# Kernel optimization log

Hardware: AMD Instinct MI355X
Metric: run time of the kernel (lower is better)

Reference implementation:

```python
import jax, jax.numpy as jnp
import numpy as np

T, B, C, H = 2048, 2, 1024, 16
D = C // H
SCALE = D ** -0.5
WSTD = C ** -0.5  # keep activations O(1) so softmax is not saturated


def setup_inputs() -> dict:
    key = jax.random.key(0)
    ks = jax.random.split(key, 6)
    return {
        "x": jax.random.normal(ks[0], (T, B, C), dtype=jnp.float32),
        "wq": jax.random.normal(ks[1], (C, C), dtype=jnp.float32) * WSTD,
        "wk": jax.random.normal(ks[2], (C, C), dtype=jnp.float32) * WSTD,
        "wv": jax.random.normal(ks[3], (C, C), dtype=jnp.float32) * WSTD,
        "wo": jax.random.normal(ks[4], (C, C), dtype=jnp.float32) * WSTD,
        "bo": jax.random.normal(ks[5], (C,), dtype=jnp.float32) * 0.02,
    }


def reference(x, wq, wk, wv, wo, bo):
    t, b, c = x.shape
    x2 = x.reshape(t * b, c)
    # SelfAttentionLinears: q scaled by head_dim^-0.5 inside the addmm
    q = (x2 @ wq) * SCALE
    k = x2 @ wk
    v = x2 @ wv
    # fairseq layout: (T, B*H, D) -> (B*H, T, D)
    q = q.reshape(t, b * H, D).transpose(1, 0, 2)
    k = k.reshape(t, b * H, D).transpose(1, 0, 2)
    v = v.reshape(t, b * H, D).transpose(1, 0, 2)
    # strided_bmm1: scores [B*H, T, T]
    scores = jnp.einsum('bqd,bkd->bqk', q, k)
    attn = jax.nn.softmax(scores, axis=-1)
    # strided_bmm2: context [B*H, T, D]
    ctx = jnp.einsum('bqk,bkd->bqd', attn, v)
    out = ctx.transpose(1, 0, 2).reshape(t, b, c)
    return out @ wo + bo
```

## Files before the change

kernel.cpp:

```cpp
#include <hip/hip_runtime.h>
#include <math.h>

#define T_DIM 2048
#define B_DIM 2
#define C_DIM 1024
#define H_DIM 16
#define D_DIM 64
#define M_DIM (T_DIM * B_DIM)
#define SCALE_Q 0.125f

typedef short short8 __attribute__((ext_vector_type(8)));
typedef float f32x4  __attribute__((ext_vector_type(4)));
typedef unsigned short ushort_t;

__device__ __forceinline__ unsigned short f2bf(float f) {
    unsigned int u = __builtin_bit_cast(unsigned int, f);
    u += 0x7FFFu + ((u >> 16) & 1u);
    return (unsigned short)(u >> 16);
}

__device__ __forceinline__ void gl_lds16(const void* g, void* l) {
    __builtin_amdgcn_global_load_lds(
        (const __attribute__((address_space(1))) void*)g,
        (__attribute__((address_space(3))) void*)l, 16, 0, 0);
}

__global__ __launch_bounds__(256) void prep(
    const float* __restrict__ x,
    const float* __restrict__ wq, const float* __restrict__ wk,
    const float* __restrict__ wv, const float* __restrict__ wo,
    ushort_t* __restrict__ xb,
    ushort_t* __restrict__ wqkv_t, ushort_t* __restrict__ wo_t)
{
    __shared__ float tile[64][65];
    const int tid = threadIdx.x;
    const int z   = blockIdx.z;

    if (z == 4) {
        const size_t base =
            ((size_t)(blockIdx.y * 16 + blockIdx.x)) * 16384 + (size_t)tid * 8;
#pragma unroll
        for (int j = 0; j < 8; ++j) {
            const size_t i = base + (size_t)j * 2048;
            const float4 v0 = *(const float4*)&x[i];
            const float4 v1 = *(const float4*)&x[i + 4];
            ushort_t o[8] = {f2bf(v0.x), f2bf(v0.y), f2bf(v0.z), f2bf(v0.w),
                             f2bf(v1.x), f2bf(v1.y), f2bf(v1.z), f2bf(v1.w)};
            *(uint4*)&xb[i] = *(uint4*)o;
        }
        return;
    }

    const int k0 = blockIdx.x * 64;
    const int n0 = blockIdx.y * 64;
    const float* src = (z == 0) ? wq : (z == 1) ? wk : (z == 2) ? wv : wo;
    ushort_t* dst = (z < 3) ? (wqkv_t + (size_t)z * C_DIM * C_DIM) : wo_t;

    const int r = tid >> 4;
    const int c = (tid & 15) * 4;
#pragma unroll
    for (int i = 0; i < 4; ++i) {
        const float4 v = *(const float4*)&src[(size_t)(k0 + r + i * 16) * C_DIM + n0 + c];
        *(float4*)&tile[r + i * 16][c] = v;
    }
    __syncthreads();
#pragma unroll
    for (int i = 0; i < 4; ++i) {
        const int r2 = r + i * 16;
        ushort4 o;
        o.x = f2bf(tile[c + 0][r2]); o.y = f2bf(tile[c + 1][r2]);
        o.z = f2bf(tile[c + 2][r2]); o.w = f2bf(tile[c + 3][r2]);
        *(ushort4*)&dst[(size_t)(n0 + r2) * C_DIM + k0 + c] = o;
    }
}

__global__ __launch_bounds__(256) void qkv_mfma(
    const ushort_t* __restrict__ xb, const ushort_t* __restrict__ wt,
    ushort_t* __restrict__ q_ws, ushort_t* __restrict__ k_ws,
    ushort_t* __restrict__ v_ws)
{
    __shared__ ushort_t lds[18432];
    ushort_t* As = lds;
    ushort_t* Bs = lds + 4096;

    const int tid  = threadIdx.x;
    const int n0   = blockIdx.x * 128;
    const int m0   = blockIdx.y * 128;
    const int w    = tid >> 6;
    const int lane = tid & 63;
    const int l16  = lane & 15;
    const int quad = lane >> 4;
    const int wm   = (w >> 1) * 64;
    const int wn   = (w & 1) * 64;

    const int o0 = tid * 8, o1 = o0 + 2048;
    const ushort_t* a0 = xb + (size_t)(m0 + (o0 >> 5)) * C_DIM + (o0 & 31);
    const ushort_t* a1 = xb + (size_t)(m0 + (o1 >> 5)) * C_DIM + (o1 & 31);
    const ushort_t* b0 = wt + (size_t)(n0 + (o0 >> 5)) * C_DIM + (o0 & 31);
    const ushort_t* b1 = wt + (size_t)(n0 + (o1 >> 5)) * C_DIM + (o1 & 31);

    f32x4 acc[4][4] = {};

    for (int k0 = 0; k0 < C_DIM; k0 += 32) {
        __syncthreads();
        gl_lds16(a0 + k0, As + o0);
        gl_lds16(a1 + k0, As + o1);
        gl_lds16(b0 + k0, Bs + o0);
        gl_lds16(b1 + k0, Bs + o1);
        __syncthreads();

        short8 af[4], bf[4];
#pragma unroll
        for (int mi = 0; mi < 4; ++mi)
            af[mi] = *(const short8*)&As[(wm + mi * 16 + l16) * 32 + quad * 8];
#pragma unroll
        for (int ni = 0; ni < 4; ++ni)
            bf[ni] = *(const short8*)&Bs[(wn + ni * 16 + l16) * 32 + quad * 8];
#pragma unroll
        for (int mi = 0; mi < 4; ++mi)
#pragma unroll
            for (int ni = 0; ni < 4; ++ni)
                acc[mi][ni] = __builtin_amdgcn_mfma_f32_16x16x32_bf16(
                    af[mi], bf[ni], acc[mi][ni], 0, 0, 0);
    }

    __syncthreads();
    ushort_t* Ep = lds + w * 4608;

    const int mat = n0 >> 10;
    const int cb  = (n0 & 1023) + wn;
    const int h   = cb >> 6;
    ushort_t* dst = (mat == 0) ? q_ws : (mat == 1) ? k_ws : v_ws;
    const float sc = (mat == 0) ? SCALE_Q : 1.0f;

#pragma unroll
    for (int mi = 0; mi < 4; ++mi)
#pragma unroll
        for (int ni = 0; ni < 4; ++ni)
#pragma unroll
            for (int r = 0; r < 4; ++r)
                Ep[(mi * 16 + quad * 4 + r) * 72 + ni * 16 + l16] =
                    f2bf(acc[mi][ni][r] * sc);

    const int rq = lane >> 3;
    const int c8 = (lane & 7) * 8;
#pragma unroll
    for (int p = 0; p < 8; ++p) {
        const int row = p * 8 + rq;
        const uint4 val = *(const uint4*)&Ep[row * 72 + c8];
        const int m = m0 + wm + row;
        const int t = m >> 1, b = m & 1;
        *(uint4*)&dst[((size_t)(b * H_DIM + h) * T_DIM + t) * D_DIM + c8] = val;
    }
}

__global__ __launch_bounds__(256) void v_transpose(
    const ushort_t* __restrict__ vn, ushort_t* __restrict__ vt)
{
    __shared__ ushort_t tile[64][72];
    const int tid = threadIdx.x;
    const int t0  = blockIdx.x * 64;
    const int bh  = blockIdx.y;
    const int r   = tid >> 3;
    const int c   = (tid & 7) * 8;
#pragma unroll
    for (int i = 0; i < 2; ++i)
        *(uint4*)&tile[r + i * 32][c] =
            *(const uint4*)&vn[((size_t)bh * T_DIM + t0 + r + i * 32) * D_DIM + c];
    __syncthreads();
#pragma unroll
    for (int i = 0; i < 2; ++i) {
        const int rd = r + i * 32;
        ushort_t o[8];
#pragma unroll
        for (int j = 0; j < 8; ++j) o[j] = tile[c + j][rd];
        *(uint4*)&vt[((size_t)bh * D_DIM + rd) * T_DIM + t0 + c] = *(uint4*)o;
    }
}

__global__ __launch_bounds__(256) void attn_mfma(
    const ushort_t* __restrict__ q, const ushort_t* __restrict__ k,
    const ushort_t* __restrict__ v, ushort_t* __restrict__ ctx)
{
    __shared__ ushort_t Ks [64][72];
    __shared__ ushort_t Vts[64][72];
    __shared__ ushort_t Ps [64][72];

    const int tid  = threadIdx.x;
    const int bh   = blockIdx.x;
    const int q0   = blockIdx.y * 64;
    const int w    = tid >> 6;
    const int lane = tid & 63;
    const int l16  = lane & 15;
    const int quad = lane >> 4;

    const int r0 = tid >> 3,         c80 = (tid & 7) * 8;
    const int r1 = (tid + 256) >> 3;
    const ushort_t* kbase = k + (size_t)bh * T_DIM * D_DIM;
    const ushort_t* vbase = v + (size_t)bh * D_DIM * T_DIM;

    short8 aq0, aq1;
    {
        const ushort_t* qrow = q + ((size_t)bh * T_DIM + q0 + 16 * w + l16) * D_DIM;
        aq0 = *(const short8*)(qrow + quad * 8);
        aq1 = *(const short8*)(qrow + 32 + quad * 8);
    }

    short8 vones;
#pragma unroll
    for (int j = 0; j < 8; ++j) vones[j] = (short)0x3F80;

    f32x4 O[4] = {};
    f32x4 Osum = {};

    const ushort_t* kp0 = kbase + (size_t)r0 * D_DIM + c80;
    const ushort_t* kp1 = kbase + (size_t)r1 * D_DIM + c80;
    const ushort_t* vp0 = vbase + (size_t)r0 * T_DIM + c80;
    const ushort_t* vp1 = vbase + (size_t)r1 * T_DIM + c80;
    uint4 kr0 = *(const uint4*)kp0;  kp0 += 64 * D_DIM;
    uint4 kr1 = *(const uint4*)kp1;  kp1 += 64 * D_DIM;
    uint4 vr0 = *(const uint4*)vp0;  vp0 += 64;
    uint4 vr1 = *(const uint4*)vp1;  vp1 += 64;

    const float LOG2E = 1.44269504f;
    const float SHIFT = 8.0f * 1.44269504f;

    for (int kt = 0; kt < 32; ++kt) {
        __syncthreads();
        *(uint4*)&Ks[r0][c80]  = kr0;
        *(uint4*)&Ks[r1][c80]  = kr1;
        *(uint4*)&Vts[r0][c80] = vr0;
        *(uint4*)&Vts[r1][c80] = vr1;
        if (kt + 1 < 32) {
            kr0 = *(const uint4*)kp0;  kp0 += 64 * D_DIM;
            kr1 = *(const uint4*)kp1;  kp1 += 64 * D_DIM;
            vr0 = *(const uint4*)vp0;  vp0 += 64;
            vr1 = *(const uint4*)vp1;  vp1 += 64;
        }
        __syncthreads();

        f32x4 S[4];
#pragma unroll
        for (int nt = 0; nt < 4; ++nt) {
            const short8 b0 = *(const short8*)&Ks[nt * 16 + l16][quad * 8];
            const short8 b1 = *(const short8*)&Ks[nt * 16 + l16][32 + quad * 8];
            f32x4 s = (f32x4){0.f, 0.f, 0.f, 0.f};
            s = __builtin_amdgcn_mfma_f32_16x16x32_bf16(aq0, b0, s, 0, 0, 0);
            s = __builtin_amdgcn_mfma_f32_16x16x32_bf16(aq1, b1, s, 0, 0, 0);
            S[nt] = s;
        }

#pragma unroll
        for (int nt = 0; nt < 4; ++nt)
#pragma unroll
            for (int r = 0; r < 4; ++r) {
                union { float f; ushort2 h; } cv;
                cv.f = exp2f(fmaf(S[nt][r], LOG2E, -SHIFT));
                Ps[16 * w + quad * 4 + r][nt * 16 + l16] = cv.h.y;
            }

        const short8 ap0 = *(const short8*)&Ps[16 * w + l16][quad * 8];
        const short8 ap1 = *(const short8*)&Ps[16 * w + l16][32 + quad * 8];

        Osum = __builtin_amdgcn_mfma_f32_16x16x32_bf16(ap0, vones, Osum, 0, 0, 0);
        Osum = __builtin_amdgcn_mfma_f32_16x16x32_bf16(ap1, vones, Osum, 0, 0, 0);

#pragma unroll
        for (int nt = 0; nt < 4; ++nt) {
            const short8 b0 = *(const short8*)&Vts[nt * 16 + l16][quad * 8];
            const short8 b1 = *(const short8*)&Vts[nt * 16 + l16][32 + quad * 8];
            O[nt] = __builtin_amdgcn_mfma_f32_16x16x32_bf16(ap0, b0, O[nt], 0, 0, 0);
            O[nt] = __builtin_amdgcn_mfma_f32_16x16x32_bf16(ap1, b1, O[nt], 0, 0, 0);
        }
    }

    const int b = bh >> 4;
    const int h = bh & 15;
#pragma unroll
    for (int r = 0; r < 4; ++r) {
        const float inv = 1.0f / Osum[r];
        const int row = q0 + 16 * w + quad * 4 + r;
#pragma unroll
        for (int nt = 0; nt < 4; ++nt)
            ctx[((size_t)row * B_DIM + b) * C_DIM + h * 64 + nt * 16 + l16] =
                f2bf(O[nt][r] * inv);
    }
}

__global__ __launch_bounds__(256) void out_mfma(
    const ushort_t* __restrict__ ctx, const ushort_t* __restrict__ wot,
    const float* __restrict__ bo, float* __restrict__ out)
{
    __shared__ ushort_t As[128 * 32];
    __shared__ ushort_t Bs[64 * 32];

    const int tid  = threadIdx.x;
    const int n0   = blockIdx.x * 64;
    const int m0   = blockIdx.y * 128;
    const int w    = tid >> 6;
    const int lane = tid & 63;
    const int l16  = lane & 15;
    const int quad = lane >> 4;
    const int wm   = (w >> 1) * 64;
    const int wn   = (w & 1) * 32;

    const int o0 = tid * 8, o1 = o0 + 2048;
    const ushort_t* a0 = ctx + (size_t)(m0 + (o0 >> 5)) * C_DIM + (o0 & 31);
    const ushort_t* a1 = ctx + (size_t)(m0 + (o1 >> 5)) * C_DIM + (o1 & 31);
    const ushort_t* b0 = wot + (size_t)(n0 + (o0 >> 5)) * C_DIM + (o0 & 31);

    f32x4 acc[4][2] = {};

    for (int k0 = 0; k0 < C_DIM; k0 += 32) {
        __syncthreads();
        gl_lds16(a0 + k0, As + o0);
        gl_lds16(a1 + k0, As + o1);
        gl_lds16(b0 + k0, Bs + o0);
        __syncthreads();

        short8 af[4], bf[2];
#pragma unroll
        for (int mi = 0; mi < 4; ++mi)
            af[mi] = *(const short8*)&As[(wm + mi * 16 + l16) * 32 + quad * 8];
#pragma unroll
        for (int ni = 0; ni < 2; ++ni)
            bf[ni] = *(const short8*)&Bs[(wn + ni * 16 + l16) * 32 + quad * 8];
#pragma unroll
        for (int mi = 0; mi < 4; ++mi)
#pragma unroll
            for (int ni = 0; ni < 2; ++ni)
                acc[mi][ni] = __builtin_amdgcn_mfma_f32_16x16x32_bf16(
                    af[mi], bf[ni], acc[mi][ni], 0, 0, 0);
    }

#pragma unroll
    for (int ni = 0; ni < 2; ++ni) {
        const int n = n0 + wn + ni * 16 + l16;
        const float bias = bo[n];
#pragma unroll
        for (int mi = 0; mi < 4; ++mi) {
            const int mb = m0 + wm + mi * 16 + quad * 4;
#pragma unroll
            for (int r = 0; r < 4; ++r)
                out[(size_t)(mb + r) * C_DIM + n] = acc[mi][ni][r] + bias;
        }
    }
}

extern "C" void kernel_launch(void* const* d_in, const int* in_sizes, int n_in,
                              void* d_out, int out_size, void* d_ws, size_t ws_size,
                              hipStream_t stream)
{
    const float* x  = (const float*)d_in[0];
    const float* wq = (const float*)d_in[1];
    const float* wk = (const float*)d_in[2];
    const float* wv = (const float*)d_in[3];
    const float* wo = (const float*)d_in[4];
    const float* bo = (const float*)d_in[5];
    float* out = (float*)d_out;

    const size_t CC  = (size_t)C_DIM * C_DIM;
    const size_t MC  = (size_t)M_DIM * C_DIM;
    ushort_t* xb     = (ushort_t*)d_ws;
    ushort_t* wqkv_t = xb + MC;
    ushort_t* wo_t   = wqkv_t + 3 * CC;
    ushort_t* q_ws   = wo_t + CC;
    ushort_t* k_ws   = q_ws + MC;
    ushort_t* v_nat  = k_ws + MC;
    ushort_t* v_t    = v_nat + MC;
    ushort_t* ctx    = v_t + MC;

    hipLaunchKernelGGL(prep, dim3(16, 16, 5), dim3(256), 0, stream,
                       x, wq, wk, wv, wo, xb, wqkv_t, wo_t);
    hipLaunchKernelGGL(qkv_mfma, dim3(24, 32), dim3(256), 0, stream,
                       xb, wqkv_t, q_ws, k_ws, v_nat);
    hipLaunchKernelGGL(v_transpose, dim3(32, 32), dim3(256), 0, stream,
                       v_nat, v_t);
    hipLaunchKernelGGL(attn_mfma, dim3(32, 32), dim3(256), 0, stream,
                       q_ws, k_ws, v_t, ctx);
    hipLaunchKernelGGL(out_mfma, dim3(16, 32), dim3(256), 0, stream,
                       ctx, wo_t, bo, out);
}
```

Baseline: 214.1 us.

## Deepen GEMM K-tiles, swizzle attention P tile, add MFMA priority hints

The QKV and output-projection GEMMs now load 64-wide K slices per barrier instead of 32, halving the number of sync/load rounds at the cost of doubled LDS tiles. The attention kernel XOR-swizzles the P scratch tile to reduce LDS bank conflicts on the transposed write/read. It also raises wave priority around MFMA sections and swaps the grid axes so query tiles of one head run adjacently. The larger LDS footprint may lower occupancy, and the grid swap requires the launch to match.

```diff
diff --git a/kernel.cpp b/kernel.cpp
--- a/kernel.cpp
+++ b/kernel.cpp
@@ -81,7 +81,7 @@
 {
     __shared__ ushort_t lds[18432];
     ushort_t* As = lds;
-    ushort_t* Bs = lds + 4096;
+    ushort_t* Bs = lds + 8192;
 
     const int tid  = threadIdx.x;
     const int n0   = blockIdx.x * 128;
@@ -93,35 +93,43 @@
     const int wm   = (w >> 1) * 64;
     const int wn   = (w & 1) * 64;
 
-    const int o0 = tid * 8, o1 = o0 + 2048;
-    const ushort_t* a0 = xb + (size_t)(m0 + (o0 >> 5)) * C_DIM + (o0 & 31);
-    const ushort_t* a1 = xb + (size_t)(m0 + (o1 >> 5)) * C_DIM + (o1 & 31);
-    const ushort_t* b0 = wt + (size_t)(n0 + (o0 >> 5)) * C_DIM + (o0 & 31);
-    const ushort_t* b1 = wt + (size_t)(n0 + (o1 >> 5)) * C_DIM + (o1 & 31);
+    const ushort_t* ag[4];
+    const ushort_t* bg[4];
+#pragma unroll
+    for (int i = 0; i < 4; ++i) {
+        const int oi = tid * 8 + i * 2048;
+        ag[i] = xb + (size_t)(m0 + (oi >> 6)) * C_DIM + (oi & 63);
+        bg[i] = wt + (size_t)(n0 + (oi >> 6)) * C_DIM + (oi & 63);
+    }
 
     f32x4 acc[4][4] = {};
 
-    for (int k0 = 0; k0 < C_DIM; k0 += 32) {
-        __syncthreads();
-        gl_lds16(a0 + k0, As + o0);
-        gl_lds16(a1 + k0, As + o1);
-        gl_lds16(b0 + k0, Bs + o0);
-        gl_lds16(b1 + k0, Bs + o1);
-        __syncthreads();
-
-        short8 af[4], bf[4];
-#pragma unroll
-        for (int mi = 0; mi < 4; ++mi)
-            af[mi] = *(const short8*)&As[(wm + mi * 16 + l16) * 32 + quad * 8];
-#pragma unroll
-        for (int ni = 0; ni < 4; ++ni)
-            bf[ni] = *(const short8*)&Bs[(wn + ni * 16 + l16) * 32 + quad * 8];
-#pragma unroll
-        for (int mi = 0; mi < 4; ++mi)
+    for (int k0 = 0; k0 < C_DIM; k0 += 64) {
+        __syncthreads();
+#pragma unroll
+        for (int i = 0; i < 4; ++i) {
+            const int oi = tid * 8 + i * 2048;
+            gl_lds16(ag[i] + k0, As + oi);
+            gl_lds16(bg[i] + k0, Bs + oi);
+        }
+        __syncthreads();
+
+#pragma unroll
+        for (int kk = 0; kk < 2; ++kk) {
+            short8 af[4], bf[4];
+#pragma unroll
+            for (int mi = 0; mi < 4; ++mi)
+                af[mi] = *(const short8*)&As[(wm + mi * 16 + l16) * 64 + kk * 32 + quad * 8];
 #pragma unroll
             for (int ni = 0; ni < 4; ++ni)
-                acc[mi][ni] = __builtin_amdgcn_mfma_f32_16x16x32_bf16(
-                    af[mi], bf[ni], acc[mi][ni], 0, 0, 0);
+                bf[ni] = *(const short8*)&Bs[(wn + ni * 16 + l16) * 64 + kk * 32 + quad * 8];
+#pragma unroll
+            for (int mi = 0; mi < 4; ++mi)
+#pragma unroll
+                for (int ni = 0; ni < 4; ++ni)
+                    acc[mi][ni] = __builtin_amdgcn_mfma_f32_16x16x32_bf16(
+                        af[mi], bf[ni], acc[mi][ni], 0, 0, 0);
+        }
     }
 
     __syncthreads();
@@ -187,8 +195,8 @@
     __shared__ ushort_t Ps [64][72];
 
     const int tid  = threadIdx.x;
-    const int bh   = blockIdx.x;
-    const int q0   = blockIdx.y * 64;
+    const int bh   = blockIdx.y;
+    const int q0   = blockIdx.x * 64;
     const int w    = tid >> 6;
     const int lane = tid & 63;
     const int l16  = lane & 15;
@@ -224,6 +232,9 @@
 
     const float LOG2E = 1.44269504f;
     const float SHIFT = 8.0f * 1.44269504f;
+
+    const int wsw = (quad & 2) << 3;
+    const int rsw = (l16 & 8) << 1;
 
     for (int kt = 0; kt < 32; ++kt) {
         __syncthreads();
@@ -240,6 +251,7 @@
         __syncthreads();
 
         f32x4 S[4];
+        __builtin_amdgcn_s_setprio(1);
 #pragma unroll
         for (int nt = 0; nt < 4; ++nt) {
             const short8 b0 = *(const short8*)&Ks[nt * 16 + l16][quad * 8];
@@ -249,6 +261,7 @@
             s = __builtin_amdgcn_mfma_f32_16x16x32_bf16(aq1, b1, s, 0, 0, 0);
             S[nt] = s;
         }
+        __builtin_amdgcn_s_setprio(0);
 
 #pragma unroll
         for (int nt = 0; nt < 4; ++nt)
@@ -256,12 +269,13 @@
             for (int r = 0; r < 4; ++r) {
                 union { float f; ushort2 h; } cv;
                 cv.f = exp2f(fmaf(S[nt][r], LOG2E, -SHIFT));
-                Ps[16 * w + quad * 4 + r][nt * 16 + l16] = cv.h.y;
+                Ps[16 * w + quad * 4 + r][(nt * 16 + l16) ^ wsw] = cv.h.y;
             }
 
-        const short8 ap0 = *(const short8*)&Ps[16 * w + l16][quad * 8];
-        const short8 ap1 = *(const short8*)&Ps[16 * w + l16][32 + quad * 8];
-
+        const short8 ap0 = *(const short8*)&Ps[16 * w + l16][(quad * 8) ^ rsw];
+        const short8 ap1 = *(const short8*)&Ps[16 * w + l16][(32 + quad * 8) ^ rsw];
+
+        __builtin_amdgcn_s_setprio(1);
         Osum = __builtin_amdgcn_mfma_f32_16x16x32_bf16(ap0, vones, Osum, 0, 0, 0);
         Osum = __builtin_amdgcn_mfma_f32_16x16x32_bf16(ap1, vones, Osum, 0, 0, 0);
 
@@ -272,6 +286,7 @@
             O[nt] = __builtin_amdgcn_mfma_f32_16x16x32_bf16(ap0, b0, O[nt], 0, 0, 0);
             O[nt] = __builtin_amdgcn_mfma_f32_16x16x32_bf16(ap1, b1, O[nt], 0, 0, 0);
         }
+        __builtin_amdgcn_s_setprio(0);
     }
 
     const int b = bh >> 4;
@@ -291,8 +306,8 @@
     const ushort_t* __restrict__ ctx, const ushort_t* __restrict__ wot,
     const float* __restrict__ bo, float* __restrict__ out)
 {
-    __shared__ ushort_t As[128 * 32];
-    __shared__ ushort_t Bs[64 * 32];
+    __shared__ ushort_t As[128 * 64];
+    __shared__ ushort_t Bs[64 * 64];
 
     const int tid  = threadIdx.x;
     const int n0   = blockIdx.x * 64;
@@ -304,33 +319,51 @@
     const int wm   = (w >> 1) * 64;
     const int wn   = (w & 1) * 32;
 
-    const int o0 = tid * 8, o1 = o0 + 2048;
-    const ushort_t* a0 = ctx + (size_t)(m0 + (o0 >> 5)) * C_DIM + (o0 & 31);
-    const ushort_t* a1 = ctx + (size_t)(m0 + (o1 >> 5)) * C_DIM + (o1 & 31);
-    const ushort_t* b0 = wot + (size_t)(n0 + (o0 >> 5)) * C_DIM + (o0 & 31);
+    const ushort_t* ag[4];
+    const ushort_t* bg[2];
+#pragma unroll
+    for (int i = 0; i < 4; ++i) {
+        const int oi = tid * 8 + i * 2048;
+        ag[i] = ctx + (size_t)(m0 + (oi >> 6)) * C_DIM + (oi & 63);
+    }
+#pragma unroll
+    for (int i = 0; i < 2; ++i) {
+        const int oi = tid * 8 + i * 2048;
+        bg[i] = wot + (size_t)(n0 + (oi >> 6)) * C_DIM + (oi & 63);
+    }
 
     f32x4 acc[4][2] = {};
 
-    for (int k0 = 0; k0 < C_DIM; k0 += 32) {
-        __syncthreads();
-        gl_lds16(a0 + k0, As + o0);
-        gl_lds16(a1 + k0, As + o1);
-        gl_lds16(b0 + k0, Bs + o0);
-        __syncthreads();
-
-        short8 af[4], bf[2];
-#pragma unroll
-        for (int mi = 0; mi < 4; ++mi)
-            af[mi] = *(const short8*)&As[(wm + mi * 16 + l16) * 32 + quad * 8];
-#pragma unroll
-        for (int ni = 0; ni < 2; ++ni)
-            bf[ni] = *(const short8*)&Bs[(wn + ni * 16 + l16) * 32 + quad * 8];
-#pragma unroll
-        for (int mi = 0; mi < 4; ++mi)
+    for (int k0 = 0; k0 < C_DIM; k0 += 64) {
+        __syncthreads();
+#pragma unroll
+        for (int i = 0; i < 4; ++i) {
+            const int oi = tid * 8 + i * 2048;
+            gl_lds16(ag[i] + k0, As + oi);
+        }
+#pragma unroll
+        for (int i = 0; i < 2; ++i) {
+            const int oi = tid * 8 + i * 2048;
+            gl_lds16(bg[i] + k0, Bs + oi);
+        }
+        __syncthreads();
+
+#pragma unroll
+        for (int kk = 0; kk < 2; ++kk) {
+            short8 af[4], bf[2];
+#pragma unroll
+            for (int mi = 0; mi < 4; ++mi)
+                af[mi] = *(const short8*)&As[(wm + mi * 16 + l16) * 64 + kk * 32 + quad * 8];
 #pragma unroll
             for (int ni = 0; ni < 2; ++ni)
-                acc[mi][ni] = __builtin_amdgcn_mfma_f32_16x16x32_bf16(
-                    af[mi], bf[ni], acc[mi][ni], 0, 0, 0);
+                bf[ni] = *(const short8*)&Bs[(wn + ni * 16 + l16) * 64 + kk * 32 + quad * 8];
+#pragma unroll
+            for (int mi = 0; mi < 4; ++mi)
+#pragma unroll
+                for (int ni = 0; ni < 2; ++ni)
+                    acc[mi][ni] = __builtin_amdgcn_mfma_f32_16x16x32_bf16(
+                        af[mi], bf[ni], acc[mi][ni], 0, 0, 0);
+        }
     }
 
 #pragma unroll
```

Result: slower. 225.7 us (+5.4%).
